# Kernel optimization log

Hardware: AMD Instinct MI355X
Metric: run time of the kernel (lower is better)

## Reference

```python
import jax, jax.numpy as jnp
import numpy as np
import math

N_HEADS = 16

def _rope_tables(T, D, dtype):
    # inv_freq over even dims, emb = [freqs, freqs] -> [T, D]
    inv_freq = 1.0 / (10000.0 ** (jnp.arange(0, D, 2, dtype=jnp.float32) / D))
    freqs = jnp.arange(T, dtype=jnp.float32)[:, None] * inv_freq[None, :]  # [T, D/2]
    emb = jnp.concatenate([freqs, freqs], axis=-1)  # [T, D]
    return jnp.cos(emb).astype(dtype), jnp.sin(emb).astype(dtype)

def _rotate_half(x):
    d = x.shape[-1] // 2
    return jnp.concatenate([-x[..., d:], x[..., :d]], axis=-1)

def setup_inputs() -> dict:
    key = jax.random.key(0)
    ks = jax.random.split(key, 5)
    B, T, C = 2, 2048, 1024
    s = 1.0 / math.sqrt(C)
    return {
        "x": jax.random.normal(ks[0], (B, T, C), dtype=jnp.float32),
        "Wq": jax.random.normal(ks[1], (C, C), dtype=jnp.float32) * s,
        "Wk": jax.random.normal(ks[2], (C, C), dtype=jnp.float32) * s,
        "Wv": jax.random.normal(ks[3], (C, C), dtype=jnp.float32) * s,
        "Wo": jax.random.normal(ks[4], (C, C), dtype=jnp.float32) * s,
    }

def reference(x, Wq, Wk, Wv, Wo):
    B, T, C = x.shape
    H = N_HEADS
    D = C // H
    # QKV projections (torch Linear, bias=False: y = x @ W.T), split into heads
    def proj(W):
        return (x @ W.T).reshape(B, T, H, D).transpose(0, 2, 1, 3)  # [B,H,T,D]
    q, k, v = proj(Wq), proj(Wk), proj(Wv)
    # RoPE
    cos, sin = _rope_tables(T, D, x.dtype)  # [T,D] each, broadcast over B,H
    q = q * cos + _rotate_half(q) * sin
    k = k * cos + _rotate_half(k) * sin
    # scaled dot-product attention with causal mask
    scale = 1.0 / math.sqrt(D)
    attn = jnp.einsum('bhtd,bhsd->bhts', q, k) * scale  # [B,H,T,T]
    row = jnp.arange(T)[:, None]
    col = jnp.arange(T)[None, :]
    attn = jnp.where(col > row, -jnp.inf, attn)
    p = jax.nn.softmax(attn, axis=-1)
    out = jnp.einsum('bhts,bhsd->bhtd', p, v)  # [B,H,T,D]
    out = out.transpose(0, 2, 1, 3).reshape(B, T, C)
    return out @ Wo.T
```

## Files before the change

kernel.cpp:

```cpp
#include <hip/hip_runtime.h>
#include <hip/hip_bf16.h>


typedef __hip_bfloat16 bf16;
typedef __attribute__((ext_vector_type(8))) short bf16x8;
typedef __attribute__((ext_vector_type(4))) float f32x4;
typedef __attribute__((ext_vector_type(4))) short short4v;

#define MFMA16(a, b, c) __builtin_amdgcn_mfma_f32_16x16x32_bf16((a), (b), (c), 0, 0, 0)

constexpr int Bn = 2, Hn = 16, Tn = 2048, Dn = 64, Cn = 1024;
constexpr size_t NE = (size_t)Bn * Tn * Cn;
constexpr size_t WE = (size_t)Cn * Cn;
constexpr float QSCALE = 0.125f * 1.44269504088896f;

__device__ inline unsigned short bfbits(float x) {
    bf16 b = __float2bfloat16(x);
    return *(unsigned short*)&b;
}

__device__ inline bf16x8 pack8(f32x4 a, f32x4 b) {
    bf16x8 r;
#pragma unroll
    for (int i = 0; i < 4; ++i) r[i] = (short)bfbits(a[i]);
#pragma unroll
    for (int i = 0; i < 4; ++i) r[4 + i] = (short)bfbits(b[i]);
    return r;
}

__global__ __launch_bounds__(256) void convert_kernel(
    const float* __restrict__ x, const float* __restrict__ wq,
    const float* __restrict__ wk, const float* __restrict__ wv,
    const float* __restrict__ wo, bf16* __restrict__ dst)
{
    int blk = blockIdx.x;
    int lane = threadIdx.x & 63;
    int lx = lane & 15, quad = lane >> 4;
    const float* src;
    size_t doff;
    if (blk < 2048) {
        int frag = blk * 4 + (threadIdx.x >> 6);
        int mt = frag >> 5, kc = frag & 31;
        src = x + (size_t)(mt * 16 + lx) * Cn + kc * 32 + quad * 8;
        doff = (size_t)frag * 512 + lane * 8;
    } else {
        int w = (blk - 2048) >> 9, b = (blk - 2048) & 511;
        const float* s4[4] = {wq, wk, wv, wo};
        int frag = b * 4 + (threadIdx.x >> 6);
        int nb = frag >> 5, kc = frag & 31;
        src = s4[w] + (size_t)(nb * 16 + lx) * Cn + kc * 32 + quad * 8;
        doff = NE + (size_t)w * WE + (size_t)frag * 512 + lane * 8;
    }
    f32x4 a = *(const f32x4*)(src);
    f32x4 b2 = *(const f32x4*)(src + 4);
    *(bf16x8*)(dst + doff) = pack8(a, b2);
}

__global__ __launch_bounds__(256) void gemm_qkv_kernel(
    const bf16* __restrict__ Xf, const bf16* __restrict__ Wbase,
    bf16* __restrict__ Qo, bf16* __restrict__ Ko, bf16* __restrict__ Vo)
{
    const int bm = blockIdx.x, bn = blockIdx.y, wsel = blockIdx.z;
    const bf16* W = Wbase + (size_t)wsel * WE;
    const int tid  = threadIdx.x;
    const int wave = tid >> 6, lane = tid & 63;
    const int lx   = lane & 15, quad = lane >> 4;
    const int wm = wave >> 1, wn = wave & 1;

    const int mt0 = bm * 8 + wm * 4;
    const int nb0 = bn * 8 + wn * 4;
    const bf16* afrag = Xf + (size_t)mt0 * 32 * 512 + (size_t)lane * 8;
    const bf16* wfrag = W + (size_t)nb0 * 32 * 512 + (size_t)lane * 8;

    f32x4 acc[4][4] = {};
    bf16x8 acur[4], bcur[4], anxt[4], bnxt[4];
#pragma unroll
    for (int i = 0; i < 4; ++i) {
        acur[i] = *(const bf16x8*)(afrag + (size_t)i * 32 * 512);
        bcur[i] = *(const bf16x8*)(wfrag + (size_t)i * 32 * 512);
    }
    for (int kc = 0; kc < 32; ++kc) {
        if (kc < 31) {
#pragma unroll
            for (int i = 0; i < 4; ++i) {
                anxt[i] = *(const bf16x8*)(afrag + ((size_t)i * 32 + kc + 1) * 512);
                bnxt[i] = *(const bf16x8*)(wfrag + ((size_t)i * 32 + kc + 1) * 512);
            }
        }
#pragma unroll
        for (int mt = 0; mt < 4; ++mt)
#pragma unroll
            for (int nt = 0; nt < 4; ++nt)
                acc[mt][nt] = MFMA16(acur[mt], bcur[nt], acc[mt][nt]);
#pragma unroll
        for (int i = 0; i < 4; ++i) { acur[i] = anxt[i]; bcur[i] = bnxt[i]; }
    }

    const int h = bn * 2 + wn;
    if (wsel <= 1) {
#pragma unroll
        for (int mt = 0; mt < 4; ++mt)
#pragma unroll
            for (int r = 0; r < 4; ++r) {
                int mg = bm * 128 + wm * 64 + mt * 16 + quad * 4 + r;
                int t  = mg & (Tn - 1);
#pragma unroll
                for (int nt = 0; nt < 2; ++nt) {
                    int d = nt * 16 + lx;
                    float ang = (float)t * __expf(-(float)d * 0.2878231366f);
                    float c, s;
                    __sincosf(ang, &s, &c);
                    float a0 = acc[mt][nt][r], a1 = acc[mt][nt + 2][r];
                    acc[mt][nt][r]     = a0 * c - a1 * s;
                    acc[mt][nt + 2][r] = a1 * c + a0 * s;
                }
            }
    }

#pragma unroll
    for (int mt = 0; mt < 4; ++mt) {
        int mg0 = bm * 128 + wm * 64 + mt * 16 + quad * 4;
        int b = mg0 >> 11, tlo = mg0 & (Tn - 1);
        if (wsel == 0) {
#pragma unroll
            for (int nt = 0; nt < 4; ++nt)
#pragma unroll
                for (int r = 0; r < 4; ++r) {
                    int d = nt * 16 + lx;
                    Qo[((size_t)(b * Hn + h) * Tn + tlo + r) * Dn + d] =
                        __float2bfloat16(acc[mt][nt][r] * QSCALE);
                }
        } else if (wsel == 1) {
            bf16* Kf = Ko + (size_t)(b * Hn + h) * Tn * Dn;
            int c = tlo >> 6, ntk = (tlo >> 4) & 3;
#pragma unroll
            for (int nt = 0; nt < 4; ++nt) {
                size_t base = ((size_t)(c * 4 + ntk) * 2 + (nt >> 1)) * 512
                            + (size_t)((nt & 1) * 2 + (lx >> 3)) * 128
                            + (size_t)(tlo & 15) * 8 + (lx & 7);
#pragma unroll
                for (int r = 0; r < 4; ++r)
                    Kf[base + (size_t)r * 8] = __float2bfloat16(acc[mt][nt][r]);
            }
        } else {
            bf16* Vf = Vo + (size_t)(b * Hn + h) * Tn * Dn;
            int c = tlo >> 6, ksv = (tlo >> 5) & 1;
            int qv = (tlo >> 3) & 3, pos0 = tlo & 7;
#pragma unroll
            for (int nt = 0; nt < 4; ++nt) {
                short4v pk;
#pragma unroll
                for (int r = 0; r < 4; ++r) pk[r] = (short)bfbits(acc[mt][nt][r]);
                *(short4v*)&Vf[((size_t)(c * 8 + nt * 2 + ksv)) * 512
                               + (size_t)qv * 128 + (size_t)lx * 8 + pos0] = pk;
            }
        }
    }
}

__global__ __launch_bounds__(256) void gemm_out_kernel(
    const bf16* __restrict__ Af, const bf16* __restrict__ W, float* __restrict__ Out)
{
    const int bm = blockIdx.x, bn = blockIdx.y;
    const int tid  = threadIdx.x;
    const int wave = tid >> 6, lane = tid & 63;
    const int lx   = lane & 15, quad = lane >> 4;
    const int wm = wave >> 1, wn = wave & 1;

    const int mt0 = bm * 8 + wm * 4;
    const int nb0 = bn * 4 + wn * 2;
    const bf16* afrag = Af + (size_t)mt0 * 32 * 512 + (size_t)lane * 8;
    const bf16* wfrag = W + (size_t)nb0 * 32 * 512 + (size_t)lane * 8;

    f32x4 acc[4][2] = {};
    bf16x8 acur[4], bcur[2], anxt[4], bnxt[2];
#pragma unroll
    for (int i = 0; i < 4; ++i)
        acur[i] = *(const bf16x8*)(afrag + (size_t)i * 32 * 512);
#pragma unroll
    for (int i = 0; i < 2; ++i)
        bcur[i] = *(const bf16x8*)(wfrag + (size_t)i * 32 * 512);
    for (int kc = 0; kc < 32; ++kc) {
        if (kc < 31) {
#pragma unroll
            for (int i = 0; i < 4; ++i)
                anxt[i] = *(const bf16x8*)(afrag + ((size_t)i * 32 + kc + 1) * 512);
#pragma unroll
            for (int i = 0; i < 2; ++i)
                bnxt[i] = *(const bf16x8*)(wfrag + ((size_t)i * 32 + kc + 1) * 512);
        }
#pragma unroll
        for (int mt = 0; mt < 4; ++mt)
#pragma unroll
            for (int nt = 0; nt < 2; ++nt)
                acc[mt][nt] = MFMA16(acur[mt], bcur[nt], acc[mt][nt]);
#pragma unroll
        for (int i = 0; i < 4; ++i) acur[i] = anxt[i];
#pragma unroll
        for (int i = 0; i < 2; ++i) bcur[i] = bnxt[i];
    }
#pragma unroll
    for (int mt = 0; mt < 4; ++mt)
#pragma unroll
        for (int nt = 0; nt < 2; ++nt)
#pragma unroll
            for (int r = 0; r < 4; ++r) {
                int mg = bm * 128 + wm * 64 + mt * 16 + quad * 4 + r;
                int ng = bn * 64 + wn * 32 + nt * 16 + lx;
                Out[(size_t)mg * Cn + ng] = acc[mt][nt][r];
            }
}

__global__ __launch_bounds__(256) void attn_kernel(
    const bf16* __restrict__ Q, const bf16* __restrict__ K,
    const bf16* __restrict__ Vt, bf16* __restrict__ O)
{
    __shared__ unsigned short Pl[4][16 * 72];
    const int f  = blockIdx.x;
    const int bh = (f & 7) * 4 + ((f >> 3) & 3);
    const int qb = 31 - (f >> 5);
    const int tid  = threadIdx.x;
    const int wave = tid >> 6, lane = tid & 63;
    const int lx   = lane & 15, quad = lane >> 4;

    const bf16* Qh = Q  + (size_t)bh * Tn * Dn;
    const bf16* Kh = K  + (size_t)bh * Tn * Dn;
    const bf16* Vh = Vt + (size_t)bh * Tn * Dn;
    unsigned short* pw = &Pl[wave][0];

    const int qrowA = qb * 64 + wave * 16 + lx;
    bf16x8 aq0 = *(const bf16x8*)(Qh + (size_t)qrowA * Dn + quad * 8);
    bf16x8 aq1 = *(const bf16x8*)(Qh + (size_t)qrowA * Dn + 32 + quad * 8);

    bf16x8 ones;
#pragma unroll
    for (int i = 0; i < 8; ++i) ones[i] = (short)0x3F80;

    f32x4 acc_o[4] = {};
    f32x4 acc_l = {};
    const int row_local = wave * 16 + quad * 4;

    for (int c = 0; c <= qb; ++c) {
        const bf16* kc = Kh + (size_t)c * 4096 + (size_t)lane * 8;
        const bf16* vc = Vh + (size_t)c * 4096 + (size_t)lane * 8;
        f32x4 accs[4] = {};
#pragma unroll
        for (int nt = 0; nt < 4; ++nt) {
            bf16x8 k0 = *(const bf16x8*)(kc + (size_t)(nt * 2) * 512);
            bf16x8 k1 = *(const bf16x8*)(kc + (size_t)(nt * 2 + 1) * 512);
            accs[nt] = MFMA16(aq0, k0, accs[nt]);
            accs[nt] = MFMA16(aq1, k1, accs[nt]);
        }
        bf16x8 vf0[4], vf1[4];
#pragma unroll
        for (int dt = 0; dt < 4; ++dt) {
            vf0[dt] = *(const bf16x8*)(vc + (size_t)(dt * 2) * 512);
            vf1[dt] = *(const bf16x8*)(vc + (size_t)(dt * 2 + 1) * 512);
        }
        if (c < qb) {
#pragma unroll
            for (int nt = 0; nt < 4; ++nt)
#pragma unroll
                for (int r = 0; r < 4; ++r)
                    pw[(quad * 4 + r) * 72 + nt * 16 + lx] = bfbits(exp2f(accs[nt][r]));
        } else {
#pragma unroll
            for (int nt = 0; nt < 4; ++nt) {
                int keyl = nt * 16 + lx;
#pragma unroll
                for (int r = 0; r < 4; ++r) {
                    float p = (keyl > row_local + r) ? 0.0f : exp2f(accs[nt][r]);
                    pw[(quad * 4 + r) * 72 + nt * 16 + lx] = bfbits(p);
                }
            }
        }
        asm volatile("s_waitcnt lgkmcnt(0)" ::: "memory");
        bf16x8 ap0 = *(const bf16x8*)&pw[lx * 72 + quad * 8];
        bf16x8 ap1 = *(const bf16x8*)&pw[lx * 72 + 32 + quad * 8];
        acc_l = MFMA16(ap0, ones, acc_l);
        acc_l = MFMA16(ap1, ones, acc_l);
#pragma unroll
        for (int dt = 0; dt < 4; ++dt) {
            acc_o[dt] = MFMA16(ap0, vf0[dt], acc_o[dt]);
            acc_o[dt] = MFMA16(ap1, vf1[dt], acc_o[dt]);
        }
    }

    const int b = bh >> 4, h = bh & 15;
    const int mtile = b * 128 + qb * 4 + wave;
#pragma unroll
    for (int dt = 0; dt < 4; ++dt) {
        int ch = h * 64 + dt * 16 + lx;
        size_t base = ((size_t)mtile * 32 + (ch >> 5)) * 512
                    + (size_t)(((ch >> 3) & 3) * 16) * 8 + (ch & 7);
#pragma unroll
        for (int r = 0; r < 4; ++r) {
            float o = acc_o[dt][r] / acc_l[r];
            O[base + (size_t)(quad * 4 + r) * 8] = __float2bfloat16(o);
        }
    }
}

extern "C" void kernel_launch(void* const* d_in, const int* in_sizes, int n_in,
                              void* d_out, int out_size, void* d_ws, size_t ws_size,
                              hipStream_t stream)
{
    const float* x  = (const float*)d_in[0];
    const float* Wq = (const float*)d_in[1];
    const float* Wk = (const float*)d_in[2];
    const float* Wv = (const float*)d_in[3];
    const float* Wo = (const float*)d_in[4];
    float* out = (float*)d_out;

    bf16* ws = (bf16*)d_ws;
    bf16* Xf = ws;
    bf16* Wb = ws + NE;
    bf16* Qb = ws + NE + 4 * WE;
    bf16* Kb = Qb + NE;
    bf16* Vb = Kb + NE;
    bf16* Ab = Xf;

    convert_kernel<<<4096, 256, 0, stream>>>(x, Wq, Wk, Wv, Wo, ws);
    gemm_qkv_kernel<<<dim3(32, 8, 3), 256, 0, stream>>>(Xf, Wb, Qb, Kb, Vb);
    attn_kernel<<<1024, 256, 0, stream>>>(Qb, Kb, Vb, Ab);
    gemm_out_kernel<<<dim3(32, 16), 256, 0, stream>>>(Ab, Wb + 3 * WE, out);
}
```

Baseline: 179.0 us.

## Stage K/V chunks in LDS via global_load_lds and vectorize P stores

The attention kernel now copies each 64-key K and V chunk into shared memory with direct global-to-LDS loads, guarded by two block barriers, instead of having every wave fetch the same fragments from global memory separately. The P tile is written as packed 4-element vectors, using a key permutation that the V projection writer now matches when it lays out V. This cuts redundant global traffic across the four waves. The cost is two __syncthreads per chunk with no double buffering, which exposes load latency.

```diff
diff --git a/kernel.cpp b/kernel.cpp
--- a/kernel.cpp
+++ b/kernel.cpp
@@ -26,6 +26,12 @@
 #pragma unroll
     for (int i = 0; i < 4; ++i) r[4 + i] = (short)bfbits(b[i]);
     return r;
+}
+
+__device__ inline void gl_lds16(const bf16* g, unsigned short* l) {
+    __builtin_amdgcn_global_load_lds(
+        (const __attribute__((address_space(1))) void*)g,
+        (__attribute__((address_space(3))) void*)l, 16, 0, 0);
 }
 
 __global__ __launch_bounds__(256) void convert_kernel(
@@ -144,16 +150,18 @@
             }
         } else {
             bf16* Vf = Vo + (size_t)(b * Hn + h) * Tn * Dn;
-            int c = tlo >> 6, ksv = (tlo >> 5) & 1;
-            int qv = (tlo >> 3) & 3, pos0 = tlo & 7;
-#pragma unroll
-            for (int nt = 0; nt < 4; ++nt) {
-                short4v pk;
-#pragma unroll
-                for (int r = 0; r < 4; ++r) pk[r] = (short)bfbits(acc[mt][nt][r]);
-                *(short4v*)&Vf[((size_t)(c * 8 + nt * 2 + ksv)) * 512
-                               + (size_t)qv * 128 + (size_t)lx * 8 + pos0] = pk;
-            }
+            int c = tlo >> 6;
+#pragma unroll
+            for (int nt = 0; nt < 4; ++nt)
+#pragma unroll
+                for (int r = 0; r < 4; ++r) {
+                    int t = tlo + r;
+                    int s = 4 * (t & 15) + ((t >> 4) & 3);
+                    Vf[((size_t)(c * 8 + nt * 2 + (s >> 5))) * 512
+                       + (size_t)((s >> 3) & 3) * 128
+                       + (size_t)lx * 8 + (s & 7)] =
+                        __float2bfloat16(acc[mt][nt][r]);
+                }
         }
     }
 }
@@ -215,6 +223,8 @@
     const bf16* __restrict__ Q, const bf16* __restrict__ K,
     const bf16* __restrict__ Vt, bf16* __restrict__ O)
 {
+    __shared__ unsigned short Ks[4096];
+    __shared__ unsigned short Vs[4096];
     __shared__ unsigned short Pl[4][16 * 72];
     const int f  = blockIdx.x;
     const int bh = (f & 7) * 4 + ((f >> 3) & 3);
@@ -241,37 +251,42 @@
     const int row_local = wave * 16 + quad * 4;
 
     for (int c = 0; c <= qb; ++c) {
-        const bf16* kc = Kh + (size_t)c * 4096 + (size_t)lane * 8;
-        const bf16* vc = Vh + (size_t)c * 4096 + (size_t)lane * 8;
+        __syncthreads();
+#pragma unroll
+        for (int j = 0; j < 2; ++j) {
+            int base = (j * 256 + wave * 64) * 8;
+            gl_lds16(Kh + (size_t)c * 4096 + base + lane * 8, Ks + base);
+            gl_lds16(Vh + (size_t)c * 4096 + base + lane * 8, Vs + base);
+        }
+        __syncthreads();
         f32x4 accs[4] = {};
 #pragma unroll
         for (int nt = 0; nt < 4; ++nt) {
-            bf16x8 k0 = *(const bf16x8*)(kc + (size_t)(nt * 2) * 512);
-            bf16x8 k1 = *(const bf16x8*)(kc + (size_t)(nt * 2 + 1) * 512);
+            bf16x8 k0 = *(const bf16x8*)&Ks[(nt * 2) * 512 + lane * 8];
+            bf16x8 k1 = *(const bf16x8*)&Ks[(nt * 2 + 1) * 512 + lane * 8];
             accs[nt] = MFMA16(aq0, k0, accs[nt]);
             accs[nt] = MFMA16(aq1, k1, accs[nt]);
         }
-        bf16x8 vf0[4], vf1[4];
-#pragma unroll
-        for (int dt = 0; dt < 4; ++dt) {
-            vf0[dt] = *(const bf16x8*)(vc + (size_t)(dt * 2) * 512);
-            vf1[dt] = *(const bf16x8*)(vc + (size_t)(dt * 2 + 1) * 512);
-        }
         if (c < qb) {
 #pragma unroll
-            for (int nt = 0; nt < 4; ++nt)
-#pragma unroll
-                for (int r = 0; r < 4; ++r)
-                    pw[(quad * 4 + r) * 72 + nt * 16 + lx] = bfbits(exp2f(accs[nt][r]));
+            for (int r = 0; r < 4; ++r) {
+                short4v pk;
+#pragma unroll
+                for (int nt = 0; nt < 4; ++nt)
+                    pk[nt] = (short)bfbits(exp2f(accs[nt][r]));
+                *(short4v*)&pw[(quad * 4 + r) * 72 + lx * 4] = pk;
+            }
         } else {
 #pragma unroll
-            for (int nt = 0; nt < 4; ++nt) {
-                int keyl = nt * 16 + lx;
-#pragma unroll
-                for (int r = 0; r < 4; ++r) {
+            for (int r = 0; r < 4; ++r) {
+                short4v pk;
+#pragma unroll
+                for (int nt = 0; nt < 4; ++nt) {
+                    int keyl = nt * 16 + lx;
                     float p = (keyl > row_local + r) ? 0.0f : exp2f(accs[nt][r]);
-                    pw[(quad * 4 + r) * 72 + nt * 16 + lx] = bfbits(p);
+                    pk[nt] = (short)bfbits(p);
                 }
+                *(short4v*)&pw[(quad * 4 + r) * 72 + lx * 4] = pk;
             }
         }
         asm volatile("s_waitcnt lgkmcnt(0)" ::: "memory");
@@ -281,8 +296,10 @@
         acc_l = MFMA16(ap1, ones, acc_l);
 #pragma unroll
         for (int dt = 0; dt < 4; ++dt) {
-            acc_o[dt] = MFMA16(ap0, vf0[dt], acc_o[dt]);
-            acc_o[dt] = MFMA16(ap1, vf1[dt], acc_o[dt]);
+            bf16x8 v0 = *(const bf16x8*)&Vs[(dt * 2) * 512 + lane * 8];
+            bf16x8 v1 = *(const bf16x8*)&Vs[(dt * 2 + 1) * 512 + lane * 8];
+            acc_o[dt] = MFMA16(ap0, v0, acc_o[dt]);
+            acc_o[dt] = MFMA16(ap1, v1, acc_o[dt]);
         }
     }
 
```

Measured after the change: 176.8 us. Within noise of the previous version (-1.2%).
